# Kernel tuning notes

Measured on AMD Instinct MI355X. Metric: run time of the kernel, lower is better.

## Reference

```python
import jax, jax.numpy as jnp
import numpy as np

EPS = 2.0 ** (-20)  # FP16_tiny
Q_DIM = 256
M_DIM = 256
NUM_HEAD = 8
KEY_DIM = Q_DIM // NUM_HEAD   # 32 per head
VAL_DIM = M_DIM // NUM_HEAD   # 32 per head
OUT_DIM = 256
B, R, S = 1, 256, 1024


def setup_inputs() -> dict:
    key = jax.random.key(0)
    ks = jax.random.split(key, 12)
    q_data = jax.random.normal(ks[0], (B, R, S, Q_DIM), dtype=jnp.float32)
    m_data = jax.random.normal(ks[1], (B, R, S, M_DIM), dtype=jnp.float32)
    q_mask = (jax.random.uniform(ks[2], (B, R, S, 1)) > 0.1).astype(jnp.float32)
    bias = jax.random.normal(ks[3], (B, R, 1, S), dtype=jnp.float32) * 0.1
    # weights stored as [in, out] (torch Linear applies x @ W.T; equivalent math)
    gl = lambda k, i, o: jax.random.normal(k, (i, o), dtype=jnp.float32) * (6.0 / (i + o)) ** 0.5
    Wq = gl(ks[4], Q_DIM, NUM_HEAD * KEY_DIM)
    Wk = gl(ks[5], M_DIM, KEY_DIM)
    Wv = gl(ks[6], M_DIM, VAL_DIM)
    # linear_o has 'final' init (zeros) in the original; use small random for a useful baseline
    Wo = jax.random.normal(ks[7], (NUM_HEAD * VAL_DIM, OUT_DIM), dtype=jnp.float32) * 0.02
    bo = jnp.zeros((OUT_DIM,), dtype=jnp.float32)
    # linear_g: 'gating' init is W=0, b=1; use small random W for non-degenerate test
    Wg = jax.random.normal(ks[8], (Q_DIM, NUM_HEAD * VAL_DIM), dtype=jnp.float32) * 0.02
    bg = jnp.ones((NUM_HEAD * VAL_DIM,), dtype=jnp.float32)
    return {"q_data": q_data, "m_data": m_data, "q_mask": q_mask, "bias": bias,
            "Wq": Wq, "Wk": Wk, "Wv": Wv, "Wo": Wo, "bo": bo, "Wg": Wg, "bg": bg}


def reference(q_data, m_data, q_mask, bias, Wq, Wk, Wv, Wo, bo, Wg, bg):
    key_scalar = KEY_DIM ** (-0.5)
    # masked mean pool over the sequence (N_seq) axis -> [B,R,q_dim]
    q_avg = jnp.sum(q_data * q_mask, axis=-2) / (jnp.sum(q_mask, axis=-2) + EPS)
    q = (q_avg @ Wq) * key_scalar                       # [B,R,H*kd]
    q = q.reshape(q.shape[:-1] + (NUM_HEAD, KEY_DIM))    # [B,R,H,kd]
    k = m_data @ Wk                                      # [B,R,S,kd]
    v = m_data @ Wv                                      # [B,R,S,vd]
    logits = jnp.einsum('brhd,brsd->brhs', q, k) + bias  # [B,R,H,S]
    weight = jax.nn.softmax(logits, axis=-1)
    weighted_avg = jnp.einsum('brhs,brsd->brhd', weight, v)  # [B,R,H,vd]
    # gating
    g = jax.nn.sigmoid(q_data @ Wg + bg)                 # [B,R,S,H*vd]
    g = g.reshape(g.shape[:-1] + (NUM_HEAD, VAL_DIM))     # [B,R,S,H,vd]
    gated = weighted_avg[:, :, None] * g                  # [B,R,S,H,vd]
    gated = gated.reshape(gated.shape[:-2] + (NUM_HEAD * VAL_DIM,))
    out = gated @ Wo + bo                                 # [B,R,S,out_dim]
    return out
```

## Files before the change

kernel.cpp:

```cpp
#include <hip/hip_runtime.h>
#include <stdint.h>

typedef __bf16 bf16x8 __attribute__((ext_vector_type(8)));
typedef float f32x4 __attribute__((ext_vector_type(4)));
typedef unsigned short ushort8 __attribute__((ext_vector_type(8)));

#define S_DIM 1024
#define R_DIM 256
#define DMODEL 256
#define EPSV 9.5367431640625e-07f
#define ASTRIDE 264

__device__ __forceinline__ unsigned short f2bf(float f) {
  uint32_t u = __float_as_uint(f);
  u += 0x7fffu + ((u >> 16) & 1u);
  return (unsigned short)(u >> 16);
}
__device__ __forceinline__ float bf2f(unsigned short s) {
  return __uint_as_float(((uint32_t)s) << 16);
}
__device__ __forceinline__ bf16x8 ldfrag(const unsigned short* p) {
  return __builtin_bit_cast(bf16x8, *(const ushort8*)p);
}
__device__ __forceinline__ bf16x8 pack8(float4 a, float4 b) {
  ushort8 u;
  u[0] = f2bf(a.x); u[1] = f2bf(a.y); u[2] = f2bf(a.z); u[3] = f2bf(a.w);
  u[4] = f2bf(b.x); u[5] = f2bf(b.y); u[6] = f2bf(b.z); u[7] = f2bf(b.w);
  return __builtin_bit_cast(bf16x8, u);
}

__global__ __launch_bounds__(256) void pack_all_kernel(const float* __restrict__ Wk,
                                                       const float* __restrict__ Wv,
                                                       const float* __restrict__ Wg,
                                                       const float* __restrict__ Wo,
                                                       unsigned short* __restrict__ wkv,
                                                       unsigned short* __restrict__ wg_p,
                                                       unsigned short* __restrict__ wo_p) {
  int bid = blockIdx.x;
  int tid = threadIdx.x;
  if (bid < 64) {
    int idx = bid * 256 + tid;
    int j = idx & 7, lane = (idx >> 3) & 63, t = idx >> 9;
    int ct = t & 3, kstep = t >> 2;
    int k = kstep * 32 + ((lane >> 4) << 3) + j;
    int col = ct * 16 + (lane & 15);
    float w = (col < 32) ? Wk[k * 32 + col] : Wv[k * 32 + (col - 32)];
    wkv[idx] = f2bf(w);
  } else {
    const float* W = (bid < 320) ? Wg : Wo;
    unsigned short* out = (bid < 320) ? wg_p : wo_p;
    int idx = ((bid < 320) ? (bid - 64) : (bid - 320)) * 256 + tid;
    int j = idx & 7, lane = (idx >> 3) & 63, t = idx >> 9;
    int ct = t & 15, kstep = t >> 4;
    int k = kstep * 32 + ((lane >> 4) << 3) + j;
    int col = ct * 16 + (lane & 15);
    out[idx] = f2bf(W[k * 256 + col]);
  }
}

template <int USE_ECHO>
__global__ __launch_bounds__(256) void streams_kernel(const float* __restrict__ m_data,
                                                      const unsigned short* __restrict__ wkv,
                                                      unsigned short* __restrict__ kb,
                                                      unsigned short* __restrict__ vb_t,
                                                      const float* __restrict__ q_data,
                                                      const float* __restrict__ q_mask,
                                                      float* __restrict__ psum,
                                                      float* __restrict__ pmask,
                                                      unsigned short* __restrict__ qb16) {
  __shared__ float mlds[256];
  __shared__ float wred[4];
  int bid = blockIdx.x;
  int tid = threadIdx.x;
  if (bid < 4096) {
    int wave = tid >> 6, lane = tid & 63;
    int g = lane >> 4, lr = lane & 15;
    int row0 = bid * 64 + wave * 16;
    const float* arow = m_data + (size_t)(row0 + lr) * DMODEL;
    f32x4 acc[4] = {};
    #pragma unroll
    for (int ks = 0; ks < 8; ks++) {
      const float4* ap = (const float4*)(arow + ks * 32 + g * 8);
      bf16x8 af = pack8(ap[0], ap[1]);
      #pragma unroll
      for (int ct = 0; ct < 4; ct++) {
        bf16x8 bf = ldfrag(&wkv[((ks * 4 + ct) << 9) + lane * 8]);
        acc[ct] = __builtin_amdgcn_mfma_f32_16x16x32_bf16(af, bf, acc[ct], 0, 0, 0);
      }
    }
    #pragma unroll
    for (int ct = 0; ct < 4; ct++) {
      #pragma unroll
      for (int rg = 0; rg < 4; rg++) {
        int row = row0 + g * 4 + rg;
        int col = ct * 16 + lr;
        unsigned short hv = f2bf(acc[ct][rg]);
        if (col < 32) {
          kb[(size_t)row * 32 + col] = hv;
        } else {
          int ra = row >> 10, sl = row & 1023;
          vb_t[((size_t)(ra * 32) + (col - 32)) * S_DIM + sl] = hv;
        }
      }
    }
  } else {
    int b2 = bid - 4096;
    int r = b2 >> 2, c = b2 & 3;
    int s0 = c * 256;
    float m = q_mask[r * S_DIM + s0 + tid];
    mlds[tid] = m;
    float ms = m;
    for (int off = 32; off; off >>= 1) ms += __shfl_down(ms, off);
    if ((tid & 63) == 0) wred[tid >> 6] = ms;
    __syncthreads();
    if (tid == 0) pmask[r * 4 + c] = wred[0] + wred[1] + wred[2] + wred[3];
    float acc = 0.f;
    size_t rowbase = (size_t)(r * S_DIM + s0);
    const float* base = q_data + rowbase * DMODEL + tid;
    if (USE_ECHO) {
      unsigned short* eb = qb16 + rowbase * DMODEL + tid;
      #pragma unroll 4
      for (int s = 0; s < 256; s++) {
        float v = base[(size_t)s * DMODEL];
        acc += v * mlds[s];
        eb[(size_t)s * DMODEL] = f2bf(v);
      }
    } else {
      #pragma unroll 4
      for (int s = 0; s < 256; s++) acc += base[(size_t)s * DMODEL] * mlds[s];
    }
    psum[(r * 4 + c) * 256 + tid] = acc;
  }
}

__global__ __launch_bounds__(256) void attn2_kernel(const unsigned short* __restrict__ kb,
                                                    const unsigned short* __restrict__ vb_t,
                                                    const float* __restrict__ psum,
                                                    const float* __restrict__ pmask,
                                                    const float* __restrict__ Wq,
                                                    const float* __restrict__ bias,
                                                    float* __restrict__ wavg) {
  int r = blockIdx.x, tid = threadIdx.x;
  int w = tid >> 6, lane = tid & 63, g = lane >> 4, lr = lane & 15;
  __shared__ float qa[256];
  __shared__ float qsp[8 * 33];
  __shared__ float lgp[8 * 1028];
  __shared__ float paccL[8 * 64 * 4];
  __shared__ float denom[8];
  float s4 = psum[(r * 4 + 0) * 256 + tid] + psum[(r * 4 + 1) * 256 + tid] +
             psum[(r * 4 + 2) * 256 + tid] + psum[(r * 4 + 3) * 256 + tid];
  float msum = pmask[r * 4] + pmask[r * 4 + 1] + pmask[r * 4 + 2] + pmask[r * 4 + 3];
  qa[tid] = s4 / (msum + EPSV);
  __syncthreads();
  float qacc = 0.f;
  #pragma unroll 8
  for (int d = 0; d < 256; d++) qacc += qa[d] * Wq[d * 256 + tid];
  qsp[(tid >> 5) * 33 + (tid & 31)] = qacc * 0.17677669529663687f;
  __syncthreads();
  ushort8 uq;
  #pragma unroll
  for (int j = 0; j < 8; j++)
    uq[j] = (lr < 8) ? f2bf(qsp[lr * 33 + g * 8 + j]) : (unsigned short)0;
  bf16x8 qf = __builtin_bit_cast(bf16x8, uq);
  for (int i = 0; i < 16; i++) {
    int rt = w * 16 + i;
    bf16x8 af = ldfrag(&kb[((size_t)r * S_DIM + rt * 16 + lr) * 32 + g * 8]);
    f32x4 d4 = {};
    d4 = __builtin_amdgcn_mfma_f32_16x16x32_bf16(af, qf, d4, 0, 0, 0);
    if (lr < 8) {
      #pragma unroll
      for (int rg = 0; rg < 4; rg++) {
        int sv = rt * 16 + g * 4 + rg;
        lgp[lr * 1028 + sv] = d4[rg] + bias[r * S_DIM + sv];
      }
    }
  }
  __syncthreads();
  for (int hh = 0; hh < 2; hh++) {
    int h = w * 2 + hh;
    float mx = -1e30f;
    #pragma unroll
    for (int i = 0; i < 16; i++) mx = fmaxf(mx, lgp[h * 1028 + lane + i * 64]);
    for (int off = 32; off; off >>= 1) mx = fmaxf(mx, __shfl_xor(mx, off));
    float sum = 0.f;
    #pragma unroll
    for (int i = 0; i < 16; i++) {
      float e = __expf(lgp[h * 1028 + lane + i * 64] - mx);
      lgp[h * 1028 + lane + i * 64] = e;
      sum += e;
    }
    for (int off = 32; off; off >>= 1) sum += __shfl_xor(sum, off);
    if (lane == 0) denom[h] = sum;
  }
  __syncthreads();
  f32x4 pv[2] = {};
  for (int kk = 0; kk < 8; kk++) {
    int ks = w * 8 + kk;
    bf16x8 pa;
    if (lr < 8) {
      const float4* pp = (const float4*)&lgp[lr * 1028 + ks * 32 + g * 8];
      pa = pack8(*(const float4*)&pp[0], *(const float4*)&pp[1]);
    } else {
      pa = __builtin_bit_cast(bf16x8, (ushort8)(unsigned short)0);
    }
    #pragma unroll
    for (int ct = 0; ct < 2; ct++) {
      bf16x8 vf = ldfrag(&vb_t[((size_t)(r * 32) + ct * 16 + lr) * S_DIM + ks * 32 + g * 8]);
      pv[ct] = __builtin_amdgcn_mfma_f32_16x16x32_bf16(pa, vf, pv[ct], 0, 0, 0);
    }
  }
  *(f32x4*)&paccL[((w * 2 + 0) * 64 + lane) * 4] = pv[0];
  *(f32x4*)&paccL[((w * 2 + 1) * 64 + lane) * 4] = pv[1];
  __syncthreads();
  {
    int h = tid >> 5, d = tid & 31;
    int ct = d >> 4, l2 = (h >> 2) * 16 + (d & 15), rg = h & 3;
    float sum = 0.f;
    #pragma unroll
    for (int w4 = 0; w4 < 4; w4++) sum += paccL[((w4 * 2 + ct) * 64 + l2) * 4 + rg];
    wavg[r * 256 + tid] = __fdividef(sum, denom[h]);
  }
}

template <int USE_BF16>
__global__ __launch_bounds__(512, 4) void gate3_kernel(const float* __restrict__ q_data,
                                                       const unsigned short* __restrict__ qb16,
                                                       const unsigned short* __restrict__ wg,
                                                       const unsigned short* __restrict__ wo,
                                                       const float* __restrict__ bgv,
                                                       const float* __restrict__ bov,
                                                       const float* __restrict__ wavg,
                                                       float* __restrict__ outp) {
  __shared__ unsigned short AsG[64 * ASTRIDE];
  __shared__ float wavs[256];
  __shared__ float bgs[256];
  __shared__ float bos[256];
  int bid = blockIdx.x;
  int r = bid >> 4, sc = bid & 15;
  int tid = threadIdx.x;
  int wave = tid >> 6, lane = tid & 63, g = lane >> 4, lr = lane & 15;
  int row0g = r * S_DIM + sc * 64;
  if (tid < 256) {
    wavs[tid] = wavg[r * 256 + tid];
    bgs[tid] = bgv[tid];
    bos[tid] = bov[tid];
  }
  #pragma unroll
  for (int i = 0; i < 4; i++) {
    int c = i * 512 + tid;
    int ra = c >> 5, cc = c & 31;
    ushort8 v;
    if (USE_BF16) {
      v = *(const ushort8*)&qb16[(size_t)(row0g + ra) * DMODEL + cc * 8];
    } else {
      const float4* p = (const float4*)&q_data[(size_t)(row0g + ra) * DMODEL + cc * 8];
      v = __builtin_bit_cast(ushort8, pack8(p[0], p[1]));
    }
    *(ushort8*)&AsG[ra * ASTRIDE + cc * 8] = v;
  }
  __syncthreads();
  f32x4 acc[4][2] = {};
  for (int ks = 0; ks < 8; ks++) {
    bf16x8 b0 = ldfrag(&wg[((ks * 16 + 2 * wave) << 9) + lane * 8]);
    bf16x8 b1 = ldfrag(&wg[((ks * 16 + 2 * wave + 1) << 9) + lane * 8]);
    bf16x8 af[4];
    #pragma unroll
    for (int rt = 0; rt < 4; rt++)
      af[rt] = ldfrag(&AsG[(rt * 16 + lr) * ASTRIDE + ks * 32 + g * 8]);
    #pragma unroll
    for (int rt = 0; rt < 4; rt++) {
      acc[rt][0] = __builtin_amdgcn_mfma_f32_16x16x32_bf16(af[rt], b0, acc[rt][0], 0, 0, 0);
      acc[rt][1] = __builtin_amdgcn_mfma_f32_16x16x32_bf16(af[rt], b1, acc[rt][1], 0, 0, 0);
    }
  }
  __syncthreads();
  #pragma unroll
  for (int rt = 0; rt < 4; rt++) {
    #pragma unroll
    for (int c0 = 0; c0 < 2; c0++) {
      int col = (wave * 2 + c0) * 16 + lr;
      float wv = wavs[col];
      float bgc = bgs[col];
      #pragma unroll
      for (int rg = 0; rg < 4; rg++) {
        int row = rt * 16 + g * 4 + rg;
        float x = acc[rt][c0][rg] + bgc;
        float sg = __fdividef(1.0f, 1.0f + __expf(-x));
        AsG[row * ASTRIDE + col] = f2bf(sg * wv);
      }
    }
  }
  __syncthreads();
  f32x4 acc2[4][2] = {};
  for (int ks = 0; ks < 8; ks++) {
    bf16x8 b0 = ldfrag(&wo[((ks * 16 + 2 * wave) << 9) + lane * 8]);
    bf16x8 b1 = ldfrag(&wo[((ks * 16 + 2 * wave + 1) << 9) + lane * 8]);
    bf16x8 af[4];
    #pragma unroll
    for (int rt = 0; rt < 4; rt++)
      af[rt] = ldfrag(&AsG[(rt * 16 + lr) * ASTRIDE + ks * 32 + g * 8]);
    #pragma unroll
    for (int rt = 0; rt < 4; rt++) {
      acc2[rt][0] = __builtin_amdgcn_mfma_f32_16x16x32_bf16(af[rt], b0, acc2[rt][0], 0, 0, 0);
      acc2[rt][1] = __builtin_amdgcn_mfma_f32_16x16x32_bf16(af[rt], b1, acc2[rt][1], 0, 0, 0);
    }
  }
  #pragma unroll
  for (int rt = 0; rt < 4; rt++) {
    #pragma unroll
    for (int c0 = 0; c0 < 2; c0++) {
      int col = (wave * 2 + c0) * 16 + lr;
      float boc = bos[col];
      #pragma unroll
      for (int rg = 0; rg < 4; rg++) {
        int row = rt * 16 + g * 4 + rg;
        outp[(size_t)(row0g + row) * DMODEL + col] = acc2[rt][c0][rg] + boc;
      }
    }
  }
}

extern "C" void kernel_launch(void* const* d_in, const int* in_sizes, int n_in,
                              void* d_out, int out_size, void* d_ws, size_t ws_size,
                              hipStream_t stream) {
  const float* q_data = (const float*)d_in[0];
  const float* m_data = (const float*)d_in[1];
  const float* q_mask = (const float*)d_in[2];
  const float* bias   = (const float*)d_in[3];
  const float* Wq     = (const float*)d_in[4];
  const float* Wk     = (const float*)d_in[5];
  const float* Wv     = (const float*)d_in[6];
  const float* Wo     = (const float*)d_in[7];
  const float* bo     = (const float*)d_in[8];
  const float* Wg     = (const float*)d_in[9];
  const float* bg     = (const float*)d_in[10];
  float* outp = (float*)d_out;

  char* ws = (char*)d_ws;
  unsigned short* kb      = (unsigned short*)(ws + 0);
  unsigned short* vb_t    = (unsigned short*)(ws + 16777216);
  unsigned short* wkv     = (unsigned short*)(ws + 33554432);
  unsigned short* wg_pack = (unsigned short*)(ws + 33587200);
  unsigned short* wo_pack = (unsigned short*)(ws + 33718272);
  float* psum  = (float*)(ws + 33849344);
  float* pmask = (float*)(ws + 34897920);
  float* wavg  = (float*)(ws + 35164160);
  const size_t QB16_OFF = 35651584;
  const size_t QB16_BYTES = (size_t)R_DIM * S_DIM * DMODEL * 2;
  bool use_echo = ws_size >= QB16_OFF + QB16_BYTES;
  unsigned short* qb16 = use_echo ? (unsigned short*)(ws + QB16_OFF) : nullptr;

  pack_all_kernel<<<576, 256, 0, stream>>>(Wk, Wv, Wg, Wo, wkv, wg_pack, wo_pack);
  if (use_echo)
    streams_kernel<1><<<5120, 256, 0, stream>>>(m_data, wkv, kb, vb_t, q_data, q_mask, psum, pmask, qb16);
  else
    streams_kernel<0><<<5120, 256, 0, stream>>>(m_data, wkv, kb, vb_t, q_data, q_mask, psum, pmask, nullptr);
  attn2_kernel<<<256, 256, 0, stream>>>(kb, vb_t, psum, pmask, Wq, bias, wavg);
  if (use_echo)
    gate3_kernel<1><<<4096, 512, 0, stream>>>(q_data, qb16, wg_pack, wo_pack, bg, bo, wavg, outp);
  else
    gate3_kernel<0><<<4096, 512, 0, stream>>>(q_data, nullptr, wg_pack, wo_pack, bg, bo, wavg, outp);
}
```

Baseline: 328.1 us.

## Stage m_data tile and K/V outputs through LDS for coalesced access

The K/V projection blocks now load their 64-row m_data tile cooperatively into LDS as bf16, using fully coalesced float4 reads, instead of each lane reading strided rows. The MFMA results are also written to an LDS buffer and then stored as 16-byte vectors. K goes out row-contiguous and V is transposed so each store covers 8 consecutive sequence positions. This replaces scattered 2-byte global stores, which matter most for the transposed V, at the cost of extra LDS traffic, two barriers and about 43KB of shared memory per block, which may reduce occupancy.

```diff
diff --git a/kernel.cpp b/kernel.cpp
--- a/kernel.cpp
+++ b/kernel.cpp
@@ -10,6 +10,7 @@
 #define DMODEL 256
 #define EPSV 9.5367431640625e-07f
 #define ASTRIDE 264
+#define OSTRIDE 72
 
 __device__ __forceinline__ unsigned short f2bf(float f) {
   uint32_t u = __float_as_uint(f);
@@ -68,20 +69,27 @@
                                                       float* __restrict__ psum,
                                                       float* __restrict__ pmask,
                                                       unsigned short* __restrict__ qb16) {
-  __shared__ float mlds[256];
-  __shared__ float wred[4];
+  __shared__ __align__(16) char smem_raw[64 * ASTRIDE * 2 + 64 * OSTRIDE * 2];
   int bid = blockIdx.x;
   int tid = threadIdx.x;
   if (bid < 4096) {
+    unsigned short* As = (unsigned short*)smem_raw;
+    unsigned short* O  = (unsigned short*)(smem_raw + 64 * ASTRIDE * 2);
     int wave = tid >> 6, lane = tid & 63;
     int g = lane >> 4, lr = lane & 15;
-    int row0 = bid * 64 + wave * 16;
-    const float* arow = m_data + (size_t)(row0 + lr) * DMODEL;
+    int row0 = bid * 64;
+    #pragma unroll
+    for (int i = 0; i < 8; i++) {
+      int c = i * 256 + tid;
+      int ra = c >> 5, cc = c & 31;
+      const float4* p = (const float4*)&m_data[(size_t)(row0 + ra) * DMODEL + cc * 8];
+      *(ushort8*)&As[ra * ASTRIDE + cc * 8] = __builtin_bit_cast(ushort8, pack8(p[0], p[1]));
+    }
+    __syncthreads();
     f32x4 acc[4] = {};
     #pragma unroll
     for (int ks = 0; ks < 8; ks++) {
-      const float4* ap = (const float4*)(arow + ks * 32 + g * 8);
-      bf16x8 af = pack8(ap[0], ap[1]);
+      bf16x8 af = ldfrag(&As[(wave * 16 + lr) * ASTRIDE + ks * 32 + g * 8]);
       #pragma unroll
       for (int ct = 0; ct < 4; ct++) {
         bf16x8 bf = ldfrag(&wkv[((ks * 4 + ct) << 9) + lane * 8]);
@@ -92,18 +100,26 @@
     for (int ct = 0; ct < 4; ct++) {
       #pragma unroll
       for (int rg = 0; rg < 4; rg++) {
-        int row = row0 + g * 4 + rg;
-        int col = ct * 16 + lr;
-        unsigned short hv = f2bf(acc[ct][rg]);
-        if (col < 32) {
-          kb[(size_t)row * 32 + col] = hv;
-        } else {
-          int ra = row >> 10, sl = row & 1023;
-          vb_t[((size_t)(ra * 32) + (col - 32)) * S_DIM + sl] = hv;
-        }
-      }
+        O[(wave * 16 + g * 4 + rg) * OSTRIDE + ct * 16 + lr] = f2bf(acc[ct][rg]);
+      }
+    }
+    __syncthreads();
+    {
+      int rowl = tid >> 2, c8 = (tid & 3) * 8;
+      ushort8 v = *(const ushort8*)&O[rowl * OSTRIDE + c8];
+      *(ushort8*)&kb[(size_t)(row0 + rowl) * 32 + c8] = v;
+    }
+    {
+      int d = tid >> 3, s8 = (tid & 7) * 8;
+      ushort8 v;
+      #pragma unroll
+      for (int j = 0; j < 8; j++) v[j] = O[(s8 + j) * OSTRIDE + 32 + d];
+      int ra = row0 >> 10, sl0 = row0 & 1023;
+      *(ushort8*)&vb_t[((size_t)(ra * 32) + d) * S_DIM + sl0 + s8] = v;
     }
   } else {
+    float* mlds = (float*)smem_raw;
+    float* wred = (float*)(smem_raw + 256 * 4);
     int b2 = bid - 4096;
     int r = b2 >> 2, c = b2 & 3;
     int s0 = c * 256;
```

Result: no change. 333.0 us (+1.5%).
